# Kernel tuning notes

Measured on AMD Instinct MI355X. Metric: run time of the kernel, lower is better.

Reference implementation:

```python
import jax, jax.numpy as jnp
import numpy as np

B, S, D, H = 2, 2048, 1024, 16
HD = D // H
SCALE = HD ** -0.5


def setup_inputs() -> dict:
    key = jax.random.key(0)
    ks = jax.random.split(key, 11)
    std = 1.0 / np.sqrt(D)
    inp = {
        'query': jax.random.normal(ks[0], (B, S, D), jnp.float32),
        'key':   jax.random.normal(ks[1], (B, S, D), jnp.float32),
        'value': jax.random.normal(ks[2], (B, S, D), jnp.float32),
        'Wq': jax.random.uniform(ks[3], (D, D), jnp.float32, -std, std),
        'bq': jax.random.uniform(ks[4], (D,), jnp.float32, -std, std),
        'Wk': jax.random.uniform(ks[5], (D, D), jnp.float32, -std, std),
        'bk': jax.random.uniform(ks[6], (D,), jnp.float32, -std, std),
        'Wv': jax.random.uniform(ks[7], (D, D), jnp.float32, -std, std),
        'bv': jax.random.uniform(ks[8], (D,), jnp.float32, -std, std),
        'Wo': jax.random.uniform(ks[9], (D, D), jnp.float32, -std, std),
        'bo': jax.random.uniform(ks[10], (D,), jnp.float32, -std, std),
    }
    return inp


def reference(query, key, value, Wq, bq, Wk, bk, Wv, bv, Wo, bo):
    # Projections (torch Linear: x @ W.T + b; here W stored as [in, out])
    def split_heads(x):  # [B,S,D] -> [B,H,S,hd]
        return x.reshape(B, S, H, HD).transpose(0, 2, 1, 3)
    Q = split_heads(query @ Wq + bq)
    K = split_heads(key @ Wk + bk)
    V = split_heads(value @ Wv + bv)
    scores = jnp.einsum('bhqd,bhkd->bhqk', Q, K) * SCALE
    attn_weights = jax.nn.softmax(scores, axis=-1)
    # dropout is identity in eval mode
    ctx = jnp.einsum('bhqk,bhkd->bhqd', attn_weights, V)
    ctx = ctx.transpose(0, 2, 1, 3).reshape(B, S, D)
    output = ctx @ Wo + bo
    return output, attn_weights
```

## Files before the change

### kernel.cpp

```cpp
#include <hip/hip_runtime.h>
#include <hip/hip_bf16.h>

typedef __attribute__((ext_vector_type(4)))  float  f32x4;
typedef __attribute__((ext_vector_type(16))) float  f32x16;
typedef __attribute__((ext_vector_type(4)))  float  floatv4;
typedef __attribute__((ext_vector_type(8)))  short  short8;
typedef __attribute__((ext_vector_type(8)))  __bf16 bf16x8;

#define NB 2
#define NS 2048
#define ND 1024
#define NH 16
#define NHD 64
#define NM (NB*NS)
#define Q_SCALE 0.18033688011112042f

#if __has_builtin(__builtin_amdgcn_exp2f)
#define EXP2(x) __builtin_amdgcn_exp2f(x)
#else
#define EXP2(x) exp2f(x)
#endif

static __device__ __forceinline__ unsigned short f2bf(float f) {
  unsigned int u = __builtin_bit_cast(unsigned int, f);
  u += 0x7fffu + ((u >> 16) & 1u);
  return (unsigned short)(u >> 16);
}

static __device__ __forceinline__ f32x4 mfma16(short8 a, short8 b, f32x4 c) {
  return __builtin_amdgcn_mfma_f32_16x16x32_bf16(
      __builtin_bit_cast(bf16x8, a), __builtin_bit_cast(bf16x8, b), c, 0, 0, 0);
}
static __device__ __forceinline__ f32x16 mfma32(short8 a, short8 b, f32x16 c) {
  return __builtin_amdgcn_mfma_f32_32x32x16_bf16(
      __builtin_bit_cast(bf16x8, a), __builtin_bit_cast(bf16x8, b), c, 0, 0, 0);
}

static __device__ __forceinline__ f32x16 zero16() {
  f32x16 z;
#pragma unroll
  for (int i = 0; i < 16; ++i) z[i] = 0.f;
  return z;
}

struct TWArgs { const float* W[4]; short* Wt[4]; };

__global__ __launch_bounds__(256) void wt_kernel(TWArgs args) {
  __shared__ float tile[32][33];
  const float* W = args.W[blockIdx.z];
  short* Wt = args.Wt[blockIdx.z];
  int k0 = blockIdx.x * 32, n0 = blockIdx.y * 32;
  int tx = threadIdx.x, ty = threadIdx.y;
#pragma unroll
  for (int i = 0; i < 4; ++i)
    tile[ty + 8 * i][tx] = W[(size_t)(k0 + ty + 8 * i) * ND + n0 + tx];
  __syncthreads();
#pragma unroll
  for (int i = 0; i < 4; ++i)
    Wt[(size_t)(n0 + ty + 8 * i) * ND + k0 + tx] = (short)f2bf(tile[tx][ty + 8 * i]);
}

struct ProjArgs {
  const void* A[3]; const short* W[3]; const float* bias[3];
  void* out[3]; float scale[3]; int mode[3];
};

template<bool A_BF16>
__global__ __launch_bounds__(256, 3) void gemm_proj(ProjArgs args) {
  int z = blockIdx.y;
  const char* Abase = (const char*)args.A[z];
  const short* W = args.W[z];
  const float* bias = args.bias[z];
  float scale = args.scale[z];
  int mode = args.mode[z];

  __shared__ short As[128 * 32];
  __shared__ short Bs[128 * 32];
  int tid = threadIdx.x;
  int lane = tid & 63;
  int wave = tid >> 6;
  int wr = wave >> 1, wc = wave & 1;
  int m0 = (blockIdx.x >> 3) * 128;
  int n0 = (blockIdx.x & 7) * 128;

  int srow = tid >> 1, shalf = tid & 1;
  unsigned sbase = (unsigned)(srow * 64 + shalf * 32);
  unsigned ssw = ((unsigned)(srow & 7)) << 4;
  unsigned d1 = sbase ^ ssw, d2 = (sbase + 16u) ^ ssw;

  f32x4 acc[4][4];
#pragma unroll
  for (int i = 0; i < 4; ++i)
#pragma unroll
    for (int j = 0; j < 4; ++j) acc[i][j] = (f32x4){0.f, 0.f, 0.f, 0.f};

  for (int kt = 0; kt < 32; ++kt) {
    int k0 = kt * 32;
    if (A_BF16) {
      const short* src = (const short*)Abase + (size_t)(m0 + srow) * ND + k0 + shalf * 16;
      short8 v0 = ((const short8*)src)[0];
      short8 v1 = ((const short8*)src)[1];
      *(short8*)((char*)As + d1) = v0;
      *(short8*)((char*)As + d2) = v1;
    } else {
      const float* src = (const float*)Abase + (size_t)(m0 + srow) * ND + k0 + shalf * 16;
      floatv4 f0 = ((const floatv4*)src)[0];
      floatv4 f1 = ((const floatv4*)src)[1];
      floatv4 f2 = ((const floatv4*)src)[2];
      floatv4 f3 = ((const floatv4*)src)[3];
      short8 v0, v1;
#pragma unroll
      for (int j = 0; j < 4; ++j) { v0[j] = (short)f2bf(f0[j]); v0[4 + j] = (short)f2bf(f1[j]); }
#pragma unroll
      for (int j = 0; j < 4; ++j) { v1[j] = (short)f2bf(f2[j]); v1[4 + j] = (short)f2bf(f3[j]); }
      *(short8*)((char*)As + d1) = v0;
      *(short8*)((char*)As + d2) = v1;
    }
    {
      const short* src = W + (size_t)(n0 + srow) * ND + k0 + shalf * 16;
      short8 v0 = ((const short8*)src)[0];
      short8 v1 = ((const short8*)src)[1];
      *(short8*)((char*)Bs + d1) = v0;
      *(short8*)((char*)Bs + d2) = v1;
    }
    __syncthreads();

    short8 af[4], bfr[4];
#pragma unroll
    for (int i = 0; i < 4; ++i) {
      int row = wr * 64 + i * 16 + (lane & 15);
      unsigned bo = ((unsigned)(row * 64 + (lane >> 4) * 16)) ^ (((unsigned)(row & 7)) << 4);
      af[i] = *(const short8*)((const char*)As + bo);
      int col = wc * 64 + i * 16 + (lane & 15);
      unsigned bo2 = ((unsigned)(col * 64 + (lane >> 4) * 16)) ^ (((unsigned)(col & 7)) << 4);
      bfr[i] = *(const short8*)((const char*)Bs + bo2);
    }
#pragma unroll
    for (int i = 0; i < 4; ++i)
#pragma unroll
      for (int j = 0; j < 4; ++j)
        acc[i][j] = mfma16(af[i], bfr[j], acc[i][j]);
    __syncthreads();
  }

#pragma unroll
  for (int j = 0; j < 4; ++j) {
    int n = n0 + wc * 64 + j * 16 + (lane & 15);
    float bv = bias[n];
#pragma unroll
    for (int i = 0; i < 4; ++i) {
#pragma unroll
      for (int r = 0; r < 4; ++r) {
        int m = m0 + wr * 64 + i * 16 + (lane >> 4) * 4 + r;
        float v = (acc[i][j][r] + bv) * scale;
        if (mode == 2) {
          ((float*)args.out[z])[(size_t)m * ND + n] = v;
        } else {
          int b = m >> 11, s = m & 2047, h = n >> 6, d = n & 63;
          size_t idx = (mode == 0)
                           ? (((size_t)(b * NH + h) * NS + s) * NHD + d)
                           : (((size_t)(b * NH + h) * NHD + d) * NS + s);
          ((short*)args.out[z])[idx] = (short)f2bf(v);
        }
      }
    }
  }
}

__global__ __launch_bounds__(256, 2) void attn_kernel(
    const short* __restrict__ Qb, const short* __restrict__ Kb,
    const short* __restrict__ Vt, short* __restrict__ Cb,
    float* __restrict__ attnw) {
  __shared__ short Ks[64 * 64];
  __shared__ short Vs[64 * 64];
  __shared__ short Ps[4][32 * 64];
  int bh = blockIdx.y;
  int q0 = blockIdx.x * 128;
  int tid = threadIdx.x;
  int wave = tid >> 6, lane = tid & 63;
  int lo = lane & 31, hi = lane >> 5;
  const short* Qh = Qb + (size_t)bh * NS * NHD;
  const short* Kh = Kb + (size_t)bh * NS * NHD;
  const short* Vh = Vt + (size_t)bh * NHD * NS;
  int qw = q0 + wave * 32;

  short8 aq[4];
#pragma unroll
  for (int ks = 0; ks < 4; ++ks)
    aq[ks] = *(const short8*)(Qh + (size_t)(qw + lo) * NHD + ks * 16 + hi * 8);

  float rs[16];
#pragma unroll
  for (int r = 0; r < 16; ++r) rs[r] = 0.f;
  f32x16 c0 = zero16(), c1 = zero16();

  char* PsW = (char*)Ps[wave];

  auto stageKV = [&](int kt, bool withV) {
#pragma unroll
    for (int rr = 0; rr < 2; ++rr) {
      int c = rr * 256 + tid;
      int row = c >> 3, off = c & 7;
      unsigned dstb = ((unsigned)(row * 128 + off * 16)) ^ (((unsigned)(row & 7)) << 4);
      *(short8*)((char*)Ks + dstb) =
          *(const short8*)(Kh + (size_t)(kt * 64 + row) * NHD + off * 8);
      if (withV)
        *(short8*)((char*)Vs + dstb) =
            *(const short8*)(Vh + (size_t)row * NS + kt * 64 + off * 8);
    }
  };

  auto scores = [&](f32x16& s0, f32x16& s1) {
#pragma unroll
    for (int ks = 0; ks < 4; ++ks) {
      unsigned ko = (unsigned)(ks * 32 + hi * 16);
      unsigned sw = ((unsigned)(lo & 7)) << 4;
      short8 bk0 = *(const short8*)((const char*)Ks + (((unsigned)(lo * 128) + ko) ^ sw));
      short8 bk1 = *(const short8*)((const char*)Ks + (((unsigned)((lo + 32) * 128) + ko) ^ sw));
      s0 = mfma32(aq[ks], bk0, s0);
      s1 = mfma32(aq[ks], bk1, s1);
    }
  };

  for (int kt = 0; kt < 32; ++kt) {
    stageKV(kt, true);
    __syncthreads();
    f32x16 s0 = zero16(), s1 = zero16();
    scores(s0, s1);
#pragma unroll
    for (int r = 0; r < 16; ++r) {
      float e0 = EXP2(s0[r]);
      float e1 = EXP2(s1[r]);
      rs[r] += e0 + e1;
      int qrow = (r & 3) + 8 * (r >> 2) + 4 * hi;
      unsigned sw = ((unsigned)(qrow & 7)) << 4;
      *(short*)(PsW + (((unsigned)(qrow * 128 + lo * 2)) ^ sw)) = (short)f2bf(e0);
      *(short*)(PsW + (((unsigned)(qrow * 128 + 64 + lo * 2)) ^ sw)) = (short)f2bf(e1);
    }
    asm volatile("s_waitcnt lgkmcnt(0)" ::: "memory");
#pragma unroll
    for (int kk = 0; kk < 4; ++kk) {
      unsigned ko = (unsigned)(kk * 32 + hi * 16);
      unsigned sw = ((unsigned)(lo & 7)) << 4;
      short8 ap = *(const short8*)(PsW + (((unsigned)(lo * 128) + ko) ^ sw));
      short8 bv0 = *(const short8*)((const char*)Vs + (((unsigned)(lo * 128) + ko) ^ sw));
      short8 bv1 = *(const short8*)((const char*)Vs + (((unsigned)((lo + 32) * 128) + ko) ^ sw));
      c0 = mfma32(ap, bv0, c0);
      c1 = mfma32(ap, bv1, c1);
    }
    __syncthreads();
  }

#pragma unroll
  for (int r = 0; r < 16; ++r) {
    float v = rs[r];
    v += __shfl_xor(v, 1);
    v += __shfl_xor(v, 2);
    v += __shfl_xor(v, 4);
    v += __shfl_xor(v, 8);
    v += __shfl_xor(v, 16);
    rs[r] = v;
  }
  float inv[16];
#pragma unroll
  for (int r = 0; r < 16; ++r) inv[r] = 1.0f / rs[r];

  int b = bh >> 4, h = bh & 15;
#pragma unroll
  for (int r = 0; r < 16; ++r) {
    int q = qw + (r & 3) + 8 * (r >> 2) + 4 * hi;
    size_t base = (size_t)(b * NS + q) * ND + h * NHD;
    Cb[base + lo] = (short)f2bf(c0[r] * inv[r]);
    Cb[base + 32 + lo] = (short)f2bf(c1[r] * inv[r]);
  }

  for (int kt = 0; kt < 32; ++kt) {
    stageKV(kt, false);
    __syncthreads();
    f32x16 s0 = zero16(), s1 = zero16();
    scores(s0, s1);
#pragma unroll
    for (int r = 0; r < 16; ++r) {
      int qrow = (r & 3) + 8 * (r >> 2) + 4 * hi;
      float* arow = attnw + ((size_t)bh * NS + (qw + qrow)) * NS + kt * 64;
      arow[lo] = EXP2(s0[r]) * inv[r];
      arow[32 + lo] = EXP2(s1[r]) * inv[r];
    }
    __syncthreads();
  }
}

extern "C" void kernel_launch(void* const* d_in, const int* in_sizes, int n_in,
                              void* d_out, int out_size, void* d_ws, size_t ws_size,
                              hipStream_t stream) {
  const float* query = (const float*)d_in[0];
  const float* key = (const float*)d_in[1];
  const float* value = (const float*)d_in[2];
  const float* Wq = (const float*)d_in[3];
  const float* bq = (const float*)d_in[4];
  const float* Wk = (const float*)d_in[5];
  const float* bk = (const float*)d_in[6];
  const float* Wv = (const float*)d_in[7];
  const float* bv = (const float*)d_in[8];
  const float* Wo = (const float*)d_in[9];
  const float* bo = (const float*)d_in[10];

  float* out = (float*)d_out;
  float* attnw = out + (size_t)NB * NS * ND;

  short* Qb = (short*)d_ws;
  short* Kb = Qb + (size_t)NB * NS * ND;
  short* Vt = Kb + (size_t)NB * NS * ND;
  short* Cb = Vt + (size_t)NB * NS * ND;
  short* WtQ = Cb + (size_t)NB * NS * ND;
  short* WtK = WtQ + (size_t)ND * ND;
  short* WtV = WtK + (size_t)ND * ND;
  short* WtO = WtV + (size_t)ND * ND;

  TWArgs tw;
  tw.W[0] = Wq; tw.W[1] = Wk; tw.W[2] = Wv; tw.W[3] = Wo;
  tw.Wt[0] = WtQ; tw.Wt[1] = WtK; tw.Wt[2] = WtV; tw.Wt[3] = WtO;
  wt_kernel<<<dim3(32, 32, 4), dim3(32, 8), 0, stream>>>(tw);

  ProjArgs pa;
  pa.A[0] = query; pa.A[1] = key; pa.A[2] = value;
  pa.W[0] = WtQ; pa.W[1] = WtK; pa.W[2] = WtV;
  pa.bias[0] = bq; pa.bias[1] = bk; pa.bias[2] = bv;
  pa.out[0] = Qb; pa.out[1] = Kb; pa.out[2] = Vt;
  pa.scale[0] = Q_SCALE; pa.scale[1] = 1.f; pa.scale[2] = 1.f;
  pa.mode[0] = 0; pa.mode[1] = 0; pa.mode[2] = 1;
  gemm_proj<false><<<dim3(256, 3), dim3(256), 0, stream>>>(pa);

  attn_kernel<<<dim3(16, 32), dim3(256), 0, stream>>>(Qb, Kb, Vt, Cb, attnw);

  ProjArgs po;
  po.A[0] = Cb; po.A[1] = Cb; po.A[2] = Cb;
  po.W[0] = WtO; po.W[1] = WtO; po.W[2] = WtO;
  po.bias[0] = bo; po.bias[1] = bo; po.bias[2] = bo;
  po.out[0] = out; po.out[1] = out; po.out[2] = out;
  po.scale[0] = 1.f; po.scale[1] = 1.f; po.scale[2] = 1.f;
  po.mode[0] = 2; po.mode[1] = 2; po.mode[2] = 2;
  gemm_proj<true><<<dim3(256, 1), dim3(256), 0, stream>>>(po);
}
```

Measured before the change: 795.3 us.

## Double-buffer K/V tiles in attention with register prefetch; use native bf16 convert

The attention kernel now keeps two shared-memory buffers for K and V and prefetches the next tile into registers while the current tile is processed. This hides global-load latency behind the MFMA and exp work of each iteration. The manual round-to-nearest bf16 conversion is replaced with the compiler's native __bf16 cast, which may map to a hardware conversion instruction. In exchange, shared memory per block grows by 16 KB, the prefetch registers add register pressure, and occupancy at two blocks per CU could be affected.

```diff
diff --git a/kernel.cpp b/kernel.cpp
--- a/kernel.cpp
+++ b/kernel.cpp
@@ -12,7 +12,6 @@
 #define ND 1024
 #define NH 16
 #define NHD 64
-#define NM (NB*NS)
 #define Q_SCALE 0.18033688011112042f
 
 #if __has_builtin(__builtin_amdgcn_exp2f)
@@ -21,10 +20,8 @@
 #define EXP2(x) exp2f(x)
 #endif
 
-static __device__ __forceinline__ unsigned short f2bf(float f) {
-  unsigned int u = __builtin_bit_cast(unsigned int, f);
-  u += 0x7fffu + ((u >> 16) & 1u);
-  return (unsigned short)(u >> 16);
+static __device__ __forceinline__ short bfc(float f) {
+  return __builtin_bit_cast(short, (__bf16)f);
 }
 
 static __device__ __forceinline__ f32x4 mfma16(short8 a, short8 b, f32x4 c) {
@@ -57,7 +54,7 @@
   __syncthreads();
 #pragma unroll
   for (int i = 0; i < 4; ++i)
-    Wt[(size_t)(n0 + ty + 8 * i) * ND + k0 + tx] = (short)f2bf(tile[tx][ty + 8 * i]);
+    Wt[(size_t)(n0 + ty + 8 * i) * ND + k0 + tx] = bfc(tile[tx][ty + 8 * i]);
 }
 
 struct ProjArgs {
@@ -110,9 +107,9 @@
       floatv4 f3 = ((const floatv4*)src)[3];
       short8 v0, v1;
 #pragma unroll
-      for (int j = 0; j < 4; ++j) { v0[j] = (short)f2bf(f0[j]); v0[4 + j] = (short)f2bf(f1[j]); }
-#pragma unroll
-      for (int j = 0; j < 4; ++j) { v1[j] = (short)f2bf(f2[j]); v1[4 + j] = (short)f2bf(f3[j]); }
+      for (int j = 0; j < 4; ++j) { v0[j] = bfc(f0[j]); v0[4 + j] = bfc(f1[j]); }
+#pragma unroll
+      for (int j = 0; j < 4; ++j) { v1[j] = bfc(f2[j]); v1[4 + j] = bfc(f3[j]); }
       *(short8*)((char*)As + d1) = v0;
       *(short8*)((char*)As + d2) = v1;
     }
@@ -160,7 +157,7 @@
           size_t idx = (mode == 0)
                            ? (((size_t)(b * NH + h) * NS + s) * NHD + d)
                            : (((size_t)(b * NH + h) * NHD + d) * NS + s);
-          ((short*)args.out[z])[idx] = (short)f2bf(v);
+          ((short*)args.out[z])[idx] = bfc(v);
         }
       }
     }
@@ -171,8 +168,8 @@
     const short* __restrict__ Qb, const short* __restrict__ Kb,
     const short* __restrict__ Vt, short* __restrict__ Cb,
     float* __restrict__ attnw) {
-  __shared__ short Ks[64 * 64];
-  __shared__ short Vs[64 * 64];
+  __shared__ short Ks[2][64 * 64];
+  __shared__ short Vs[2][64 * 64];
   __shared__ short Ps[4][32 * 64];
   int bh = blockIdx.y;
   int q0 = blockIdx.x * 128;
@@ -196,37 +193,48 @@
 
   char* PsW = (char*)Ps[wave];
 
-  auto stageKV = [&](int kt, bool withV) {
-#pragma unroll
-    for (int rr = 0; rr < 2; ++rr) {
-      int c = rr * 256 + tid;
-      int row = c >> 3, off = c & 7;
-      unsigned dstb = ((unsigned)(row * 128 + off * 16)) ^ (((unsigned)(row & 7)) << 4);
-      *(short8*)((char*)Ks + dstb) =
-          *(const short8*)(Kh + (size_t)(kt * 64 + row) * NHD + off * 8);
-      if (withV)
-        *(short8*)((char*)Vs + dstb) =
-            *(const short8*)(Vh + (size_t)row * NS + kt * 64 + off * 8);
+  int srow = tid >> 3, soff = tid & 7;
+  unsigned dst0 = ((unsigned)(srow * 128 + soff * 16)) ^ (((unsigned)(srow & 7)) << 4);
+  unsigned dst1 = ((unsigned)((srow + 32) * 128 + soff * 16)) ^ (((unsigned)((srow + 32) & 7)) << 4);
+
+  short8 kA, kB, vA, vB;
+  auto loadKV = [&](int kt, bool withV) {
+    kA = *(const short8*)(Kh + (size_t)(kt * 64 + srow) * NHD + soff * 8);
+    kB = *(const short8*)(Kh + (size_t)(kt * 64 + srow + 32) * NHD + soff * 8);
+    if (withV) {
+      vA = *(const short8*)(Vh + (size_t)srow * NS + kt * 64 + soff * 8);
+      vB = *(const short8*)(Vh + (size_t)(srow + 32) * NS + kt * 64 + soff * 8);
     }
   };
-
-  auto scores = [&](f32x16& s0, f32x16& s1) {
+  auto writeKV = [&](int cur, bool withV) {
+    *(short8*)((char*)Ks[cur] + dst0) = kA;
+    *(short8*)((char*)Ks[cur] + dst1) = kB;
+    if (withV) {
+      *(short8*)((char*)Vs[cur] + dst0) = vA;
+      *(short8*)((char*)Vs[cur] + dst1) = vB;
+    }
+  };
+
+  auto scores = [&](int cur, f32x16& s0, f32x16& s1) {
 #pragma unroll
     for (int ks = 0; ks < 4; ++ks) {
       unsigned ko = (unsigned)(ks * 32 + hi * 16);
       unsigned sw = ((unsigned)(lo & 7)) << 4;
-      short8 bk0 = *(const short8*)((const char*)Ks + (((unsigned)(lo * 128) + ko) ^ sw));
-      short8 bk1 = *(const short8*)((const char*)Ks + (((unsigned)((lo + 32) * 128) + ko) ^ sw));
+      short8 bk0 = *(const short8*)((const char*)Ks[cur] + (((unsigned)(lo * 128) + ko) ^ sw));
+      short8 bk1 = *(const short8*)((const char*)Ks[cur] + (((unsigned)((lo + 32) * 128) + ko) ^ sw));
       s0 = mfma32(aq[ks], bk0, s0);
       s1 = mfma32(aq[ks], bk1, s1);
     }
   };
 
+  loadKV(0, true);
   for (int kt = 0; kt < 32; ++kt) {
-    stageKV(kt, true);
+    int cur = kt & 1;
+    writeKV(cur, true);
+    if (kt + 1 < 32) loadKV(kt + 1, true);
     __syncthreads();
     f32x16 s0 = zero16(), s1 = zero16();
-    scores(s0, s1);
+    scores(cur, s0, s1);
 #pragma unroll
     for (int r = 0; r < 16; ++r) {
       float e0 = EXP2(s0[r]);
@@ -234,8 +242,8 @@
       rs[r] += e0 + e1;
       int qrow = (r & 3) + 8 * (r >> 2) + 4 * hi;
       unsigned sw = ((unsigned)(qrow & 7)) << 4;
-      *(short*)(PsW + (((unsigned)(qrow * 128 + lo * 2)) ^ sw)) = (short)f2bf(e0);
-      *(short*)(PsW + (((unsigned)(qrow * 128 + 64 + lo * 2)) ^ sw)) = (short)f2bf(e1);
+      *(short*)(PsW + (((unsigned)(qrow * 128 + lo * 2)) ^ sw)) = bfc(e0);
+      *(short*)(PsW + (((unsigned)(qrow * 128 + 64 + lo * 2)) ^ sw)) = bfc(e1);
     }
     asm volatile("s_waitcnt lgkmcnt(0)" ::: "memory");
 #pragma unroll
@@ -243,8 +251,8 @@
       unsigned ko = (unsigned)(kk * 32 + hi * 16);
       unsigned sw = ((unsigned)(lo & 7)) << 4;
       short8 ap = *(const short8*)(PsW + (((unsigned)(lo * 128) + ko) ^ sw));
-      short8 bv0 = *(const short8*)((const char*)Vs + (((unsigned)(lo * 128) + ko) ^ sw));
-      short8 bv1 = *(const short8*)((const char*)Vs + (((unsigned)((lo + 32) * 128) + ko) ^ sw));
+      short8 bv0 = *(const short8*)((const char*)Vs[cur] + (((unsigned)(lo * 128) + ko) ^ sw));
+      short8 bv1 = *(const short8*)((const char*)Vs[cur] + (((unsigned)((lo + 32) * 128) + ko) ^ sw));
       c0 = mfma32(ap, bv0, c0);
       c1 = mfma32(ap, bv1, c1);
     }
@@ -270,15 +278,18 @@
   for (int r = 0; r < 16; ++r) {
     int q = qw + (r & 3) + 8 * (r >> 2) + 4 * hi;
     size_t base = (size_t)(b * NS + q) * ND + h * NHD;
-    Cb[base + lo] = (short)f2bf(c0[r] * inv[r]);
-    Cb[base + 32 + lo] = (short)f2bf(c1[r] * inv[r]);
-  }
-
+    Cb[base + lo] = bfc(c0[r] * inv[r]);
+    Cb[base + 32 + lo] = bfc(c1[r] * inv[r]);
+  }
+
+  loadKV(0, false);
   for (int kt = 0; kt < 32; ++kt) {
-    stageKV(kt, false);
+    int cur = kt & 1;
+    writeKV(cur, false);
+    if (kt + 1 < 32) loadKV(kt + 1, false);
     __syncthreads();
     f32x16 s0 = zero16(), s1 = zero16();
-    scores(s0, s1);
+    scores(cur, s0, s1);
 #pragma unroll
     for (int r = 0; r < 16; ++r) {
       int qrow = (r & 3) + 8 * (r >> 2) + 4 * hi;
```

After: 765.8 us. 3.7% less time.
